# Performance work log

Measured on AMD Instinct MI355X. Metric: run time of the kernel, lower is better.

Reference implementation:

```python
import jax, jax.numpy as jnp
import numpy as np
from jax import lax

NO_STEPS = 32


def make_identity_grid(D, H, W, dtype=jnp.float32):
    # matches learnsim init_identity_grid_3d: [1, D, H, W, 3] with last dim (x, y, z)
    xs = jnp.linspace(-1.0, 1.0, W, dtype=dtype)
    ys = jnp.linspace(-1.0, 1.0, H, dtype=dtype)
    zs = jnp.linspace(-1.0, 1.0, D, dtype=dtype)
    gz, gy, gx = jnp.meshgrid(zs, ys, xs, indexing='ij')  # each [D, H, W]
    return jnp.stack([gx, gy, gz], axis=-1)[None]  # [1, D, H, W, 3]


def grid_sample_3d(vol, grid):
    # vol: [N, C, D, H, W]; grid: [N, D, H, W, 3] normalized (x,y,z)
    # trilinear, padding_mode='border', align_corners=True
    N, C, D, H, W = vol.shape
    ix = jnp.clip((grid[..., 0] + 1.0) * 0.5 * (W - 1), 0.0, W - 1)
    iy = jnp.clip((grid[..., 1] + 1.0) * 0.5 * (H - 1), 0.0, H - 1)
    iz = jnp.clip((grid[..., 2] + 1.0) * 0.5 * (D - 1), 0.0, D - 1)
    x0f, y0f, z0f = jnp.floor(ix), jnp.floor(iy), jnp.floor(iz)
    fx, fy, fz = ix - x0f, iy - y0f, iz - z0f  # fractional weights [N,D,H,W]
    x0 = x0f.astype(jnp.int32); y0 = y0f.astype(jnp.int32); z0 = z0f.astype(jnp.int32)
    x1 = jnp.minimum(x0 + 1, W - 1)
    y1 = jnp.minimum(y0 + 1, H - 1)
    z1 = jnp.minimum(z0 + 1, D - 1)

    def sample_one(vol_b, z0b, z1b, y0b, y1b, x0b, x1b, fxb, fyb, fzb):
        vflat = vol_b.reshape(C, -1)  # [C, D*H*W]
        def g(zi, yi, xi):
            idx = (zi * H + yi) * W + xi
            return jnp.take(vflat, idx.reshape(-1), axis=1).reshape(C, D, H, W)
        wx0, wy0, wz0 = 1.0 - fxb, 1.0 - fyb, 1.0 - fzb
        out = (g(z0b, y0b, x0b) * (wz0 * wy0 * wx0)
             + g(z0b, y0b, x1b) * (wz0 * wy0 * fxb)
             + g(z0b, y1b, x0b) * (wz0 * fyb * wx0)
             + g(z0b, y1b, x1b) * (wz0 * fyb * fxb)
             + g(z1b, y0b, x0b) * (fzb * wy0 * wx0)
             + g(z1b, y0b, x1b) * (fzb * wy0 * fxb)
             + g(z1b, y1b, x0b) * (fzb * fyb * wx0)
             + g(z1b, y1b, x1b) * (fzb * fyb * fxb))
        return out

    return jax.vmap(sample_one)(vol, z0, z1, y0, y1, x0, x1, fx, fy, fz)


def setup_inputs() -> dict:
    key = jax.random.key(0)
    N, C, D, H, W = 2, 3, 128, 128, 128
    v = jax.random.normal(key, (N, C, D, H, W), dtype=jnp.float32)
    identity_grid = make_identity_grid(D, H, W)
    return {"v": v, "identity_grid": identity_grid}


def reference(v, identity_grid):
    # scaling-and-squaring integration of a stationary velocity field
    N = v.shape[0]
    disp0 = v / jnp.asarray(2.0 ** NO_STEPS, v.dtype)

    def step(disp, _):
        # [N, D, H, W, 3] warp grid
        transformation = identity_grid + jnp.transpose(disp, (0, 2, 3, 4, 1))
        disp = disp + grid_sample_3d(disp, transformation)
        return disp, None

    displacement, _ = lax.scan(step, disp0, None, length=NO_STEPS)
    transformation = jnp.transpose(identity_grid, (0, 4, 1, 2, 3)) + displacement
    return (transformation, displacement)
```

## Files before the change

kernel.cpp:

```cpp
#include <hip/hip_runtime.h>


#define NSTEPS 32

constexpr int Dd = 128, Hh = 128, Ww = 128, Nb = 2, Cc = 3;
constexpr int VOX = Dd * Hh * Ww;
constexpr int NV  = Nb * VOX;
constexpr int THREADS = 256;

__global__ __launch_bounds__(THREADS) void svf_init(const float* __restrict__ v,
                                                    float4* __restrict__ A) {
    int i = blockIdx.x * THREADS + threadIdx.x;
    int n = i >> 21;
    int s = i & (VOX - 1);
    const float sc = 2.3283064365386963e-10f;
    int b = n * Cc * VOX + s;
    float dx = v[b]           * sc;
    float dy = v[b + VOX]     * sc;
    float dz = v[b + 2 * VOX] * sc;
    A[i] = make_float4(dx, dy, dz, 0.0f);
}

__global__ __launch_bounds__(THREADS) void svf_step(const float4* __restrict__ src,
                                                    float4* __restrict__ dst,
                                                    const float* __restrict__ idg) {
    int i = blockIdx.x * THREADS + threadIdx.x;
    int s = i & (VOX - 1);
    int base = i - s;

    float4 d = src[i];
    float id_x = idg[3 * s + 0];
    float id_y = idg[3 * s + 1];
    float id_z = idg[3 * s + 2];

    float ix = ((id_x + d.x) + 1.0f) * 0.5f * 127.0f;
    float iy = ((id_y + d.y) + 1.0f) * 0.5f * 127.0f;
    float iz = ((id_z + d.z) + 1.0f) * 0.5f * 127.0f;
    ix = fminf(fmaxf(ix, 0.0f), 127.0f);
    iy = fminf(fmaxf(iy, 0.0f), 127.0f);
    iz = fminf(fmaxf(iz, 0.0f), 127.0f);

    float x0f = floorf(ix), y0f = floorf(iy), z0f = floorf(iz);
    float fx = ix - x0f, fy = iy - y0f, fz = iz - z0f;
    int x0 = (int)x0f, y0 = (int)y0f, z0 = (int)z0f;
    int x1 = min(x0 + 1, 127);
    int y1 = min(y0 + 1, 127);
    int z1 = min(z0 + 1, 127);

    float wx0 = 1.0f - fx, wy0 = 1.0f - fy, wz0 = 1.0f - fz;

    int r00 = base + (z0 << 14) + (y0 << 7);
    int r01 = base + (z0 << 14) + (y1 << 7);
    int r10 = base + (z1 << 14) + (y0 << 7);
    int r11 = base + (z1 << 14) + (y1 << 7);

    float4 g000 = src[r00 + x0];
    float4 g001 = src[r00 + x1];
    float4 g010 = src[r01 + x0];
    float4 g011 = src[r01 + x1];
    float4 g100 = src[r10 + x0];
    float4 g101 = src[r10 + x1];
    float4 g110 = src[r11 + x0];
    float4 g111 = src[r11 + x1];

    float w000 = wz0 * wy0 * wx0;
    float w001 = wz0 * wy0 * fx;
    float w010 = wz0 * fy  * wx0;
    float w011 = wz0 * fy  * fx;
    float w100 = fz  * wy0 * wx0;
    float w101 = fz  * wy0 * fx;
    float w110 = fz  * fy  * wx0;
    float w111 = fz  * fy  * fx;

    float ox = g000.x * w000 + g001.x * w001 + g010.x * w010 + g011.x * w011
             + g100.x * w100 + g101.x * w101 + g110.x * w110 + g111.x * w111;
    float oy = g000.y * w000 + g001.y * w001 + g010.y * w010 + g011.y * w011
             + g100.y * w100 + g101.y * w101 + g110.y * w110 + g111.y * w111;
    float oz = g000.z * w000 + g001.z * w001 + g010.z * w010 + g011.z * w011
             + g100.z * w100 + g101.z * w101 + g110.z * w110 + g111.z * w111;

    dst[i] = make_float4(d.x + ox, d.y + oy, d.z + oz, 0.0f);
}

__global__ __launch_bounds__(THREADS) void svf_final(const float4* __restrict__ A,
                                                     const float* __restrict__ idg,
                                                     float* __restrict__ out) {
    int i = blockIdx.x * THREADS + threadIdx.x;
    int n = i >> 21;
    int s = i & (VOX - 1);
    float4 d = A[i];
    float id_x = idg[3 * s + 0];
    float id_y = idg[3 * s + 1];
    float id_z = idg[3 * s + 2];

    int ob = n * Cc * VOX + s;
    out[ob]            = id_x + d.x;
    out[ob + VOX]      = id_y + d.y;
    out[ob + 2 * VOX]  = id_z + d.z;
    float* disp_out = out + (size_t)Nb * Cc * VOX;
    disp_out[ob]           = d.x;
    disp_out[ob + VOX]     = d.y;
    disp_out[ob + 2 * VOX] = d.z;
}

extern "C" void kernel_launch(void* const* d_in, const int* in_sizes, int n_in,
                              void* d_out, int out_size, void* d_ws, size_t ws_size,
                              hipStream_t stream) {
    const float* v   = (const float*)d_in[0];
    const float* idg = (const float*)d_in[1];
    float* out = (float*)d_out;

    float4* A = (float4*)d_ws;
    float4* B = (float4*)d_out;

    dim3 grid(NV / THREADS), block(THREADS);

    svf_init<<<grid, block, 0, stream>>>(v, A);
    for (int k = 0; k < NSTEPS; ++k) {
        const float4* src = (k & 1) ? (const float4*)B : (const float4*)A;
        float4*       dst = (k & 1) ? A : B;
        svf_step<<<grid, block, 0, stream>>>(src, dst, idg);
    }
    svf_final<<<grid, block, 0, stream>>>(A, idg, out);
}
```

Before: 1.680 ms.

## Replace identity-grid reads with per-axis tables and swizzle blocks across XCDs

The identity grid is separable, so its three coordinates are pulled into a 384-entry device table once, and the step and final kernels index that table by x, y and z. This removes a 24 MB strided read of the full identity grid on every step. The step kernel also remaps block IDs so that each of the eight XCDs handles one contiguous range of voxels, which is meant to improve L2 locality for the gather reads. The table depends on the identity grid being exactly separable, which holds for the linspace meshgrid input.

```diff
diff --git a/kernel.cpp b/kernel.cpp
--- a/kernel.cpp
+++ b/kernel.cpp
@@ -7,6 +7,17 @@
 constexpr int VOX = Dd * Hh * Ww;
 constexpr int NV  = Nb * VOX;
 constexpr int THREADS = 256;
+constexpr int NBLK = NV / THREADS;
+constexpr int NXCD = 8;
+
+__device__ float g_tab[3 * 128];
+
+__global__ __launch_bounds__(128) void extract_tables(const float* __restrict__ idg) {
+    int t = threadIdx.x;
+    g_tab[t]       = idg[3 * t];
+    g_tab[128 + t] = idg[3 * (t << 7) + 1];
+    g_tab[256 + t] = idg[3 * (t << 14) + 2];
+}
 
 __global__ __launch_bounds__(THREADS) void svf_init(const float* __restrict__ v,
                                                     float4* __restrict__ A) {
@@ -22,16 +33,21 @@
 }
 
 __global__ __launch_bounds__(THREADS) void svf_step(const float4* __restrict__ src,
-                                                    float4* __restrict__ dst,
-                                                    const float* __restrict__ idg) {
-    int i = blockIdx.x * THREADS + threadIdx.x;
+                                                    float4* __restrict__ dst) {
+    int bid = blockIdx.x;
+    int swz = (bid & (NXCD - 1)) * (NBLK / NXCD) + (bid >> 3);
+    int i = swz * THREADS + threadIdx.x;
     int s = i & (VOX - 1);
     int base = i - s;
 
+    int xg = s & 127;
+    int yg = (s >> 7) & 127;
+    int zg = s >> 14;
+
     float4 d = src[i];
-    float id_x = idg[3 * s + 0];
-    float id_y = idg[3 * s + 1];
-    float id_z = idg[3 * s + 2];
+    float id_x = g_tab[xg];
+    float id_y = g_tab[128 + yg];
+    float id_z = g_tab[256 + zg];
 
     float ix = ((id_x + d.x) + 1.0f) * 0.5f * 127.0f;
     float iy = ((id_y + d.y) + 1.0f) * 0.5f * 127.0f;
@@ -83,15 +99,19 @@
 }
 
 __global__ __launch_bounds__(THREADS) void svf_final(const float4* __restrict__ A,
-                                                     const float* __restrict__ idg,
                                                      float* __restrict__ out) {
     int i = blockIdx.x * THREADS + threadIdx.x;
     int n = i >> 21;
     int s = i & (VOX - 1);
+
+    int xg = s & 127;
+    int yg = (s >> 7) & 127;
+    int zg = s >> 14;
+
     float4 d = A[i];
-    float id_x = idg[3 * s + 0];
-    float id_y = idg[3 * s + 1];
-    float id_z = idg[3 * s + 2];
+    float id_x = g_tab[xg];
+    float id_y = g_tab[128 + yg];
+    float id_z = g_tab[256 + zg];
 
     int ob = n * Cc * VOX + s;
     out[ob]            = id_x + d.x;
@@ -113,13 +133,14 @@
     float4* A = (float4*)d_ws;
     float4* B = (float4*)d_out;
 
-    dim3 grid(NV / THREADS), block(THREADS);
+    dim3 grid(NBLK), block(THREADS);
 
+    extract_tables<<<1, 128, 0, stream>>>(idg);
     svf_init<<<grid, block, 0, stream>>>(v, A);
     for (int k = 0; k < NSTEPS; ++k) {
         const float4* src = (k & 1) ? (const float4*)B : (const float4*)A;
         float4*       dst = (k & 1) ? A : B;
-        svf_step<<<grid, block, 0, stream>>>(src, dst, idg);
+        svf_step<<<grid, block, 0, stream>>>(src, dst);
     }
-    svf_final<<<grid, block, 0, stream>>>(A, idg, out);
+    svf_final<<<grid, block, 0, stream>>>(A, out);
 }
```

Result: faster. 1.388 ms (-17.3%).
